# Kernel optimization log

Hardware: AMD Instinct MI355X
Metric: run time of the kernel (lower is better)

## Reference

```python
import jax, jax.numpy as jnp
import numpy as np

B, T, D, H, HD = 4, 2048, 1024, 16, 64
EPS = 1e-6


def _rotary_tables(seq_len, d_head):
    n = d_head // 4
    angular_freq = (1.0 / 1024) ** jnp.linspace(0, 1, n, dtype=jnp.float32)
    angular_freq = jnp.concatenate([angular_freq, jnp.zeros((n,), jnp.float32)])  # [d_head//2]
    theta = jnp.outer(jnp.arange(seq_len, dtype=jnp.float32), angular_freq)  # [T, d_head//2]
    return jnp.cos(theta), jnp.sin(theta)


def _apply_rotary(x, cos, sin):
    # x: [B, T, H, d]
    xf = x.astype(jnp.float32)
    x1, x2 = jnp.split(xf, 2, axis=-1)
    c = cos[None, :, None, :]
    s = sin[None, :, None, :]
    y1 = x1 * c + x2 * s
    y2 = -x1 * s + x2 * c
    return jnp.concatenate([y1, y2], axis=-1).astype(x.dtype)


def _rmsnorm(x, eps):
    return x * jax.lax.rsqrt(jnp.mean(x * x, axis=-1, keepdims=True) + eps)


def setup_inputs() -> dict:
    key = jax.random.key(0)
    ks = jax.random.split(key, 5)
    scale = 1.0 / np.sqrt(D)
    x = jax.random.normal(ks[0], (B, T, D), jnp.float32)
    wq = jax.random.normal(ks[1], (D, D), jnp.float32) * scale
    wk = jax.random.normal(ks[2], (D, D), jnp.float32) * scale
    wv = jax.random.normal(ks[3], (D, D), jnp.float32) * scale
    wo = jax.random.normal(ks[4], (D, D), jnp.float32) * scale
    mask = jnp.tril(jnp.ones((T, T), dtype=bool))  # causal
    return {"x": x, "wq": wq, "wk": wk, "wv": wv, "wo": wo, "mask": mask}


def reference(x, wq, wk, wv, wo, mask):
    # QKV projections (equinox Linear: y = x @ W.T)
    q = (x @ wq.T).reshape(B, T, H, HD)
    k = (x @ wk.T).reshape(B, T, H, HD)
    v = (x @ wv.T).reshape(B, T, H, HD)
    # QK-norm (RMS norm without weight)
    q = _rmsnorm(q, EPS)
    k = _rmsnorm(k, EPS)
    # Rotary embedding
    cos, sin = _rotary_tables(T, HD)
    q = _apply_rotary(q, cos, sin)
    k = _apply_rotary(k, cos, sin)
    # Attention
    scores = jnp.einsum('bshd,bthd->bhst', q, k) / jnp.sqrt(jnp.float32(HD))
    scores = jnp.where(mask[None, None, :, :], scores, -jnp.inf)
    weights = jax.nn.softmax(scores, axis=-1)
    out = jnp.einsum('bhst,bthd->bshd', weights, v)
    out = out.reshape(B, T, D)
    return out @ wo.T
```

## Files before the change

kernel.cpp:

```cpp
#include <hip/hip_runtime.h>
#include <hip/hip_bf16.h>
#include <math.h>

#define B_ 4
#define T_ 2048
#define D_ 1024
#define H_ 16
#define HD_ 64

typedef _Float16 f16x8 __attribute__((ext_vector_type(8)));
typedef _Float16 f16x4 __attribute__((ext_vector_type(4)));
typedef float f32x4 __attribute__((ext_vector_type(4)));

__device__ __forceinline__ void gload_lds16(const _Float16* g, _Float16* l) {
    __builtin_amdgcn_global_load_lds(
        (const __attribute__((address_space(1))) void*)g,
        (__attribute__((address_space(3))) void*)l,
        16, 0, 0);
}

__global__ __launch_bounds__(256) void castf(const float* __restrict__ in,
                                             _Float16* __restrict__ out, int n4) {
    const int i = blockIdx.x * 256 + threadIdx.x;
    if (i < n4) {
        const float4 v = ((const float4*)in)[i];
        f16x4 h = {(_Float16)v.x, (_Float16)v.y, (_Float16)v.z, (_Float16)v.w};
        ((f16x4*)out)[i] = h;
    }
}

__global__ __launch_bounds__(256) void castw(const float* __restrict__ a,
                                             const float* __restrict__ b,
                                             const float* __restrict__ c,
                                             const float* __restrict__ d,
                                             _Float16* __restrict__ oa,
                                             _Float16* __restrict__ ob,
                                             _Float16* __restrict__ oc,
                                             _Float16* __restrict__ od) {
    const int z = blockIdx.z;
    const float* in = (z == 0) ? a : (z == 1 ? b : (z == 2 ? c : d));
    _Float16* out = (z == 0) ? oa : (z == 1 ? ob : (z == 2 ? oc : od));
    const int i = blockIdx.x * 256 + threadIdx.x;
    const float4 v = ((const float4*)in)[i];
    f16x4 h = {(_Float16)v.x, (_Float16)v.y, (_Float16)v.z, (_Float16)v.w};
    ((f16x4*)out)[i] = h;
}

__global__ __launch_bounds__(256) void gemm_qkv(const _Float16* __restrict__ A,
                                                const _Float16* __restrict__ Wq,
                                                const _Float16* __restrict__ Wk,
                                                const _Float16* __restrict__ Wv,
                                                _Float16* __restrict__ qh,
                                                _Float16* __restrict__ kh,
                                                _Float16* __restrict__ vt) {
    constexpr int K = D_;
    const int z = blockIdx.z;
    const _Float16* W = (z == 0) ? Wq : (z == 1 ? Wk : Wv);
    __shared__ _Float16 As[128 * 32];
    __shared__ _Float16 Bs[128 * 32];
    const int tid = threadIdx.x;
    const int lane = tid & 63, w = tid >> 6;
    const int col = lane & 15, quad = lane >> 4;
    const int wm = w >> 1, wn = w & 1;
    const int row0 = blockIdx.y * 128, col0 = blockIdx.x * 128;
    const int sr = lane >> 2, sc = (lane & 3) * 8;

    f32x4 acc[4][4];
#pragma unroll
    for (int i = 0; i < 4; ++i)
#pragma unroll
        for (int j = 0; j < 4; ++j) acc[i][j] = (f32x4){0.f, 0.f, 0.f, 0.f};

    for (int kt = 0; kt < K / 32; ++kt) {
        const int k0 = kt * 32;
#pragma unroll
        for (int it = 0; it < 2; ++it) {
            const int rb = it * 64 + w * 16;
            gload_lds16(A + (size_t)(row0 + rb + sr) * K + k0 + sc, As + rb * 32);
            gload_lds16(W + (size_t)(col0 + rb + sr) * K + k0 + sc, Bs + rb * 32);
        }
        __syncthreads();
        f16x8 af[4], bf[4];
#pragma unroll
        for (int i = 0; i < 4; ++i) {
            af[i] = *(const f16x8*)&As[(wm * 64 + i * 16 + col) * 32 + quad * 8];
            bf[i] = *(const f16x8*)&Bs[(wn * 64 + i * 16 + col) * 32 + quad * 8];
        }
#pragma unroll
        for (int mi = 0; mi < 4; ++mi)
#pragma unroll
            for (int ni = 0; ni < 4; ++ni)
                acc[mi][ni] = __builtin_amdgcn_mfma_f32_16x16x32_f16(af[mi], bf[ni],
                                                                     acc[mi][ni], 0, 0, 0);
        __syncthreads();
    }

    if (z < 2) {
        _Float16* C = (z == 0) ? qh : kh;
        const float qscale = (z == 0) ? 0.18033688011112042f : 1.0f;
        const float fr = exp2f(-10.0f * (float)col * (1.0f / 15.0f));
#pragma unroll
        for (int mi = 0; mi < 4; ++mi) {
            float ssq[4];
#pragma unroll
            for (int r = 0; r < 4; ++r) {
                float t = 0.f;
#pragma unroll
                for (int ni = 0; ni < 4; ++ni) t += acc[mi][ni][r] * acc[mi][ni][r];
                ssq[r] = t;
            }
#pragma unroll
            for (int st = 1; st < 16; st <<= 1)
#pragma unroll
                for (int r = 0; r < 4; ++r) ssq[r] += __shfl_xor(ssq[r], st, 64);
            const int rowb = row0 + wm * 64 + mi * 16 + quad * 4;
#pragma unroll
            for (int r = 0; r < 4; ++r) {
                const float scl = rsqrtf(ssq[r] * (1.0f / 64.0f) + 1e-6f) * qscale;
                const int t = (rowb + r) & (T_ - 1);
                float s, c;
                sincosf((float)t * fr, &s, &c);
                const float x0 = acc[mi][0][r] * scl;
                const float x1 = acc[mi][1][r] * scl;
                const float x2 = acc[mi][2][r] * scl;
                const float x3 = acc[mi][3][r] * scl;
                const float y0 = fmaf(x0, c, x2 * s);
                const float y2 = fmaf(x2, c, -x0 * s);
                const size_t base = (size_t)(rowb + r) * D_ + col0 + wn * 64 + col;
                C[base + 0]  = (_Float16)y0;
                C[base + 16] = (_Float16)x1;
                C[base + 32] = (_Float16)y2;
                C[base + 48] = (_Float16)x3;
            }
        }
    } else {
        const int hh = blockIdx.x * 2 + wn;
#pragma unroll
        for (int mi = 0; mi < 4; ++mi) {
            const int row = row0 + wm * 64 + mi * 16 + quad * 4;
            const int bb = row >> 11;
            const int t0m = row & (T_ - 1);
#pragma unroll
            for (int ni = 0; ni < 4; ++ni) {
                const int d = ni * 16 + col;
                f16x4 pk = {(_Float16)acc[mi][ni][0], (_Float16)acc[mi][ni][1],
                            (_Float16)acc[mi][ni][2], (_Float16)acc[mi][ni][3]};
                *(f16x4*)&vt[((size_t)(bb * H_ + hh) * HD_ + d) * T_ + t0m] = pk;
            }
        }
    }
}

__global__ __launch_bounds__(256) void gemm_wo(const _Float16* __restrict__ A,
                                               const _Float16* __restrict__ W,
                                               float* __restrict__ C) {
    constexpr int K = D_, N = D_;
    __shared__ _Float16 As[128 * 32];
    __shared__ _Float16 Bs[128 * 32];
    const int tid = threadIdx.x;
    const int lane = tid & 63, w = tid >> 6;
    const int col = lane & 15, quad = lane >> 4;
    const int wm = w >> 1, wn = w & 1;
    const int row0 = blockIdx.y * 128, col0 = blockIdx.x * 128;
    const int sr = lane >> 2, sc = (lane & 3) * 8;

    f32x4 acc[4][4];
#pragma unroll
    for (int i = 0; i < 4; ++i)
#pragma unroll
        for (int j = 0; j < 4; ++j) acc[i][j] = (f32x4){0.f, 0.f, 0.f, 0.f};

    for (int kt = 0; kt < K / 32; ++kt) {
        const int k0 = kt * 32;
#pragma unroll
        for (int it = 0; it < 2; ++it) {
            const int rb = it * 64 + w * 16;
            gload_lds16(A + (size_t)(row0 + rb + sr) * K + k0 + sc, As + rb * 32);
            gload_lds16(W + (size_t)(col0 + rb + sr) * K + k0 + sc, Bs + rb * 32);
        }
        __syncthreads();
        f16x8 af[4], bf[4];
#pragma unroll
        for (int i = 0; i < 4; ++i) {
            af[i] = *(const f16x8*)&As[(wm * 64 + i * 16 + col) * 32 + quad * 8];
            bf[i] = *(const f16x8*)&Bs[(wn * 64 + i * 16 + col) * 32 + quad * 8];
        }
#pragma unroll
        for (int mi = 0; mi < 4; ++mi)
#pragma unroll
            for (int ni = 0; ni < 4; ++ni)
                acc[mi][ni] = __builtin_amdgcn_mfma_f32_16x16x32_f16(af[mi], bf[ni],
                                                                     acc[mi][ni], 0, 0, 0);
        __syncthreads();
    }
#pragma unroll
    for (int mi = 0; mi < 4; ++mi)
#pragma unroll
        for (int ni = 0; ni < 4; ++ni)
#pragma unroll
            for (int r = 0; r < 4; ++r)
                C[(size_t)(row0 + wm * 64 + mi * 16 + quad * 4 + r) * N +
                  col0 + wn * 64 + ni * 16 + col] = acc[mi][ni][r];
}

#define LDP 88

__global__ __launch_bounds__(512) void flash_mfma(const _Float16* __restrict__ qh,
                                                  const _Float16* __restrict__ kh,
                                                  const _Float16* __restrict__ vt,
                                                  _Float16* __restrict__ o) {
    __shared__ _Float16 Kl[64 * 64];
    __shared__ _Float16 Vl[64 * 64];
    __shared__ _Float16 Pl[8][16 * LDP];
    const int tid = threadIdx.x;
    const int lane = tid & 63, w = tid >> 6;
    const int col = lane & 15, quad = lane >> 4;
    const int bh = blockIdx.x, b = bh >> 4, h = bh & 15;
    const int srow = lane >> 3;
    const int schunk = (lane & 7) ^ srow;
    const int sw = col & 7;

    for (int phase = 0; phase < 2; ++phase) {
        const int qt = (phase == 0) ? (int)blockIdx.y : (15 - (int)blockIdx.y);
        const int q0 = qt * 128;

        const int tq = q0 + w * 16 + col;
        const _Float16* qp = qh + ((size_t)(b * T_ + tq) * H_ + h) * HD_ + quad * 8;
        const f16x8 qB0 = *(const f16x8*)(qp);
        const f16x8 qB1 = *(const f16x8*)(qp + 32);

        f32x4 oa[4];
#pragma unroll
        for (int i = 0; i < 4; ++i) oa[i] = (f32x4){0.f, 0.f, 0.f, 0.f};
        float l_ = 0.f;

        const int nkt = 2 * qt + 2;
        for (int kt = 0; kt < nkt; ++kt) {
            const int k0 = kt * 64;
            {
                const int r = w * 8 + srow;
                gload_lds16(kh + ((size_t)(b * T_ + k0 + r) * H_ + h) * HD_ + schunk * 8,
                            Kl + (w * 8) * 64);
                gload_lds16(vt + ((size_t)(b * H_ + h) * HD_ + r) * T_ + k0 + schunk * 8,
                            Vl + (w * 8) * 64);
            }
            __syncthreads();

            f32x4 s[4];
#pragma unroll
            for (int tn = 0; tn < 4; ++tn) {
                const _Float16* kp = &Kl[(tn * 16 + col) * 64];
                const f16x8 kA0 = *(const f16x8*)(kp + ((quad ^ sw) << 3));
                const f16x8 kA1 = *(const f16x8*)(kp + (((quad | 4) ^ sw) << 3));
                f32x4 a = (f32x4){0.f, 0.f, 0.f, 0.f};
                a = __builtin_amdgcn_mfma_f32_16x16x32_f16(kA0, qB0, a, 0, 0, 0);
                a = __builtin_amdgcn_mfma_f32_16x16x32_f16(kA1, qB1, a, 0, 0, 0);
                s[tn] = a;
            }

            if (k0 + 63 > q0 + w * 16) {
                const int qq = q0 + w * 16 + col;
#pragma unroll
                for (int tn = 0; tn < 4; ++tn)
#pragma unroll
                    for (int r = 0; r < 4; ++r) {
                        const int key = k0 + tn * 16 + quad * 4 + r;
                        if (key > qq) s[tn][r] = -1e30f;
                    }
            }

#pragma unroll
            for (int tn = 0; tn < 4; ++tn) {
                f16x4 pk;
#pragma unroll
                for (int r = 0; r < 4; ++r) {
                    const float p = exp2f(s[tn][r]);
                    l_ += p;
                    pk[r] = (_Float16)p;
                }
                *(f16x4*)&Pl[w][col * LDP + tn * 16 + quad * 4] = pk;
            }

            const f16x8 pA0 = *(const f16x8*)&Pl[w][col * LDP + quad * 8];
            const f16x8 pA1 = *(const f16x8*)&Pl[w][col * LDP + quad * 8 + 32];
#pragma unroll
            for (int tn = 0; tn < 4; ++tn) {
                const _Float16* vp = &Vl[(tn * 16 + col) * 64];
                const f16x8 vB0 = *(const f16x8*)(vp + ((quad ^ sw) << 3));
                const f16x8 vB1 = *(const f16x8*)(vp + (((quad | 4) ^ sw) << 3));
                oa[tn] = __builtin_amdgcn_mfma_f32_16x16x32_f16(pA0, vB0, oa[tn], 0, 0, 0);
                oa[tn] = __builtin_amdgcn_mfma_f32_16x16x32_f16(pA1, vB1, oa[tn], 0, 0, 0);
            }
            __syncthreads();
        }

        l_ += __shfl_xor(l_, 16, 64);
        l_ += __shfl_xor(l_, 32, 64);
        const float linv = 1.0f / l_;
        float inv[4];
#pragma unroll
        for (int r = 0; r < 4; ++r) inv[r] = __shfl(linv, quad * 4 + r, 64);
#pragma unroll
        for (int tn = 0; tn < 4; ++tn)
#pragma unroll
            for (int r = 0; r < 4; ++r)
                o[((size_t)(b * T_ + q0 + w * 16 + quad * 4 + r) * H_ + h) * HD_ + tn * 16 + col] =
                    (_Float16)(oa[tn][r] * inv[r]);
    }
}

extern "C" void kernel_launch(void* const* d_in, const int* in_sizes, int n_in,
                              void* d_out, int out_size, void* d_ws, size_t ws_size,
                              hipStream_t stream) {
    const float* x  = (const float*)d_in[0];
    const float* wq = (const float*)d_in[1];
    const float* wk = (const float*)d_in[2];
    const float* wv = (const float*)d_in[3];
    const float* wo = (const float*)d_in[4];
    float* out = (float*)d_out;

    const size_t NE = (size_t)B_ * T_ * D_;
    const size_t WE = (size_t)D_ * D_;
    _Float16* xh  = (_Float16*)d_ws;
    _Float16* qh  = xh + NE;
    _Float16* kh  = qh + NE;
    _Float16* vth = kh + NE;
    _Float16* oh  = vth + NE;
    _Float16* wqh = oh + NE;
    _Float16* wkh = wqh + WE;
    _Float16* wvh = wkh + WE;
    _Float16* woh = wvh + WE;

    castf<<<NE / 1024, 256, 0, stream>>>(x, xh, (int)(NE / 4));
    castw<<<dim3(WE / 1024, 1, 4), 256, 0, stream>>>(wq, wk, wv, wo,
                                                     wqh, wkh, wvh, woh);

    gemm_qkv<<<dim3(D_ / 128, (B_ * T_) / 128, 3), 256, 0, stream>>>(
        xh, wqh, wkh, wvh, qh, kh, vth);

    flash_mfma<<<dim3(B_ * H_, 8, 1), 512, 0, stream>>>(qh, kh, vth, oh);

    gemm_wo<<<dim3(D_ / 128, (B_ * T_) / 128, 1), 256, 0, stream>>>(oh, woh, out);
}
```

Before: 274.8 us.

## Rewrite QKV GEMM as 256x256 tile with double-buffered LDS ping-pong schedule

Measured after the change: 289.3 us. 1.05x slower.

```diff
diff --git a/kernel.cpp b/kernel.cpp
--- a/kernel.cpp
+++ b/kernel.cpp
@@ -46,61 +46,163 @@
     ((f16x4*)out)[i] = h;
 }
 
-__global__ __launch_bounds__(256) void gemm_qkv(const _Float16* __restrict__ A,
-                                                const _Float16* __restrict__ Wq,
-                                                const _Float16* __restrict__ Wk,
-                                                const _Float16* __restrict__ Wv,
-                                                _Float16* __restrict__ qh,
-                                                _Float16* __restrict__ kh,
-                                                _Float16* __restrict__ vt) {
-    constexpr int K = D_;
+
+#define PHASE_MID() \
+    __builtin_amdgcn_s_barrier(); \
+    asm volatile("s_waitcnt lgkmcnt(0)" ::: "memory"); \
+    __builtin_amdgcn_sched_barrier(0); \
+    __builtin_amdgcn_s_setprio(1)
+
+#define PHASE_END() \
+    __builtin_amdgcn_s_setprio(0); \
+    __builtin_amdgcn_s_barrier()
+
+#define VM_PHASE_END(N) \
+    __builtin_amdgcn_s_setprio(0); \
+    __builtin_amdgcn_sched_barrier(0); \
+    asm volatile("s_waitcnt vmcnt(" #N ")" ::: "memory"); \
+    __builtin_amdgcn_sched_barrier(0); \
+    __builtin_amdgcn_s_barrier()
+
+#define LOAD_A(AR, P, MH) { \
+    _Pragma("unroll") \
+    for (int i_ = 0; i_ < 4; ++i_) { \
+        AR[i_][0] = *(const f16x8*)&As[(P) * 16384 + rowA[MH][i_] + c0s]; \
+        AR[i_][1] = *(const f16x8*)&As[(P) * 16384 + rowA[MH][i_] + c1s]; \
+    } }
+
+#define LOAD_B(P, NH) { \
+    _Pragma("unroll") \
+    for (int j_ = 0; j_ < 2; ++j_) { \
+        bF[j_][0] = *(const f16x8*)&Bs[(P) * 16384 + rowB[2 * (NH) + j_] + c0s]; \
+        bF[j_][1] = *(const f16x8*)&Bs[(P) * 16384 + rowB[2 * (NH) + j_] + c1s]; \
+    } }
+
+#define MFMA_Q(AR, MB, NH) { \
+    _Pragma("unroll") \
+    for (int i_ = 0; i_ < 4; ++i_) { \
+        _Pragma("unroll") \
+        for (int j_ = 0; j_ < 2; ++j_) { \
+            f32x4& d_ = acc[(MB) + i_][2 * (NH) + j_]; \
+            d_ = __builtin_amdgcn_mfma_f32_16x16x32_f16(AR[i_][0], bF[j_][0], d_, 0, 0, 0); \
+            d_ = __builtin_amdgcn_mfma_f32_16x16x32_f16(AR[i_][1], bF[j_][1], d_, 0, 0, 0); \
+        } } }
+
+#define STAGE_A(P, T, HH) \
+    gload_lds16(Ap + (size_t)(row0 + (HH) * 128 + w8s) * 1024 + (T) * 64 + sch, \
+                &As[(P) * 16384 + (HH) * 8192 + (w << 9)]); \
+    gload_lds16(Ap + (size_t)(row0 + (HH) * 128 + 64 + w8s) * 1024 + (T) * 64 + sch, \
+                &As[(P) * 16384 + (HH) * 8192 + 4096 + (w << 9)])
+
+#define STAGE_B(P, T, HH) \
+    gload_lds16(Wp + (size_t)(col0 + (HH) * 128 + w8s) * 1024 + (T) * 64 + sch, \
+                &Bs[(P) * 16384 + (HH) * 8192 + (w << 9)]); \
+    gload_lds16(Wp + (size_t)(col0 + (HH) * 128 + 64 + w8s) * 1024 + (T) * 64 + sch, \
+                &Bs[(P) * 16384 + (HH) * 8192 + 4096 + (w << 9)])
+
+__global__ __launch_bounds__(512, 2) void gemm_qkv(const _Float16* __restrict__ A,
+                                                   const _Float16* __restrict__ Wq,
+                                                   const _Float16* __restrict__ Wk,
+                                                   const _Float16* __restrict__ Wv,
+                                                   _Float16* __restrict__ qh,
+                                                   _Float16* __restrict__ kh,
+                                                   _Float16* __restrict__ vt) {
     const int z = blockIdx.z;
-    const _Float16* W = (z == 0) ? Wq : (z == 1 ? Wk : Wv);
-    __shared__ _Float16 As[128 * 32];
-    __shared__ _Float16 Bs[128 * 32];
+    const _Float16* Wp = (z == 0) ? Wq : (z == 1 ? Wk : Wv);
+    const _Float16* Ap = A;
+    __shared__ _Float16 As[2 * 16384];
+    __shared__ _Float16 Bs[2 * 16384];
+
     const int tid = threadIdx.x;
     const int lane = tid & 63, w = tid >> 6;
     const int col = lane & 15, quad = lane >> 4;
-    const int wm = w >> 1, wn = w & 1;
-    const int row0 = blockIdx.y * 128, col0 = blockIdx.x * 128;
-    const int sr = lane >> 2, sc = (lane & 3) * 8;
-
-    f32x4 acc[4][4];
-#pragma unroll
-    for (int i = 0; i < 4; ++i)
+    const int wr = w >> 2, wc = w & 3;
+    const int row0 = blockIdx.y * 256, col0 = blockIdx.x * 256;
+
+    const int w8s = (w << 3) + (lane >> 3);
+    const int sch = (((lane & 7) ^ (lane >> 3)) << 3);
+
+    const int swz = col & 7;
+    const int c0s = ((quad ^ swz) << 3);
+    const int c1s = (((quad | 4) ^ swz) << 3);
+
+    int rowA[2][4], rowB[4];
+#pragma unroll
+    for (int i = 0; i < 4; ++i) {
+        rowA[0][i] = (wr * 128 + i * 16 + col) * 64;
+        rowA[1][i] = rowA[0][i] + 4096;
+        rowB[i]    = (wc * 64 + i * 16 + col) * 64;
+    }
+
+    f32x4 acc[8][4];
+#pragma unroll
+    for (int i = 0; i < 8; ++i)
 #pragma unroll
         for (int j = 0; j < 4; ++j) acc[i][j] = (f32x4){0.f, 0.f, 0.f, 0.f};
 
-    for (int kt = 0; kt < K / 32; ++kt) {
-        const int k0 = kt * 32;
-#pragma unroll
-        for (int it = 0; it < 2; ++it) {
-            const int rb = it * 64 + w * 16;
-            gload_lds16(A + (size_t)(row0 + rb + sr) * K + k0 + sc, As + rb * 32);
-            gload_lds16(W + (size_t)(col0 + rb + sr) * K + k0 + sc, Bs + rb * 32);
-        }
-        __syncthreads();
-        f16x8 af[4], bf[4];
-#pragma unroll
-        for (int i = 0; i < 4; ++i) {
-            af[i] = *(const f16x8*)&As[(wm * 64 + i * 16 + col) * 32 + quad * 8];
-            bf[i] = *(const f16x8*)&Bs[(wn * 64 + i * 16 + col) * 32 + quad * 8];
-        }
-#pragma unroll
-        for (int mi = 0; mi < 4; ++mi)
-#pragma unroll
-            for (int ni = 0; ni < 4; ++ni)
-                acc[mi][ni] = __builtin_amdgcn_mfma_f32_16x16x32_f16(af[mi], bf[ni],
-                                                                     acc[mi][ni], 0, 0, 0);
-        __syncthreads();
-    }
+    f16x8 aF[4][2], aG[4][2], bF[2][2];
+
+    STAGE_A(0, 0, 0); STAGE_A(0, 0, 1);
+    STAGE_B(0, 0, 0); STAGE_B(0, 0, 1);
+    STAGE_A(1, 1, 0); STAGE_A(1, 1, 1);
+    __builtin_amdgcn_sched_barrier(0);
+    asm volatile("s_waitcnt vmcnt(4)" ::: "memory");
+    __builtin_amdgcn_sched_barrier(0);
+    __builtin_amdgcn_s_barrier();
+
+    for (int it = 0; it < 7; ++it) {
+        const int c1 = 2 * it + 1, n0 = 2 * it + 2, n1 = 2 * it + 3;
+        LOAD_A(aF, 0, 0); LOAD_B(0, 0);
+        STAGE_B(1, c1, 0);
+        PHASE_MID(); MFMA_Q(aF, 0, 0); PHASE_END();
+        LOAD_A(aG, 0, 1);
+        STAGE_B(1, c1, 1);
+        PHASE_MID(); MFMA_Q(aG, 4, 0); PHASE_END();
+        LOAD_B(0, 1);
+        STAGE_A(0, n0, 0);
+        PHASE_MID(); MFMA_Q(aG, 4, 1); PHASE_END();
+        STAGE_A(0, n0, 1);
+        PHASE_MID(); MFMA_Q(aF, 0, 1);
+        VM_PHASE_END(4);
+        LOAD_A(aF, 1, 0); LOAD_B(1, 0);
+        STAGE_B(0, n0, 0);
+        PHASE_MID(); MFMA_Q(aF, 0, 0); PHASE_END();
+        LOAD_A(aG, 1, 1);
+        STAGE_B(0, n0, 1);
+        PHASE_MID(); MFMA_Q(aG, 4, 0); PHASE_END();
+        LOAD_B(1, 1);
+        STAGE_A(1, n1, 0);
+        PHASE_MID(); MFMA_Q(aG, 4, 1); PHASE_END();
+        STAGE_A(1, n1, 1);
+        PHASE_MID(); MFMA_Q(aF, 0, 1);
+        VM_PHASE_END(4);
+    }
+
+    LOAD_A(aF, 0, 0); LOAD_B(0, 0);
+    STAGE_B(1, 15, 0);
+    PHASE_MID(); MFMA_Q(aF, 0, 0); PHASE_END();
+    LOAD_A(aG, 0, 1);
+    STAGE_B(1, 15, 1);
+    PHASE_MID(); MFMA_Q(aG, 4, 0); PHASE_END();
+    LOAD_B(0, 1);
+    PHASE_MID(); MFMA_Q(aG, 4, 1); PHASE_END();
+    PHASE_MID(); MFMA_Q(aF, 0, 1);
+    VM_PHASE_END(0);
+    LOAD_A(aF, 1, 0); LOAD_B(1, 0);
+    PHASE_MID(); MFMA_Q(aF, 0, 0); PHASE_END();
+    LOAD_A(aG, 1, 1);
+    PHASE_MID(); MFMA_Q(aG, 4, 0); PHASE_END();
+    LOAD_B(1, 1);
+    PHASE_MID(); MFMA_Q(aG, 4, 1); PHASE_END();
+    PHASE_MID(); MFMA_Q(aF, 0, 1);
+    __builtin_amdgcn_s_setprio(0);
 
     if (z < 2) {
         _Float16* C = (z == 0) ? qh : kh;
         const float qscale = (z == 0) ? 0.18033688011112042f : 1.0f;
         const float fr = exp2f(-10.0f * (float)col * (1.0f / 15.0f));
 #pragma unroll
-        for (int mi = 0; mi < 4; ++mi) {
+        for (int mi = 0; mi < 8; ++mi) {
             float ssq[4];
 #pragma unroll
             for (int r = 0; r < 4; ++r) {
@@ -113,7 +215,7 @@
             for (int st = 1; st < 16; st <<= 1)
 #pragma unroll
                 for (int r = 0; r < 4; ++r) ssq[r] += __shfl_xor(ssq[r], st, 64);
-            const int rowb = row0 + wm * 64 + mi * 16 + quad * 4;
+            const int rowb = row0 + wr * 128 + mi * 16 + quad * 4;
 #pragma unroll
             for (int r = 0; r < 4; ++r) {
                 const float scl = rsqrtf(ssq[r] * (1.0f / 64.0f) + 1e-6f) * qscale;
@@ -126,7 +228,7 @@
                 const float x3 = acc[mi][3][r] * scl;
                 const float y0 = fmaf(x0, c, x2 * s);
                 const float y2 = fmaf(x2, c, -x0 * s);
-                const size_t base = (size_t)(rowb + r) * D_ + col0 + wn * 64 + col;
+                const size_t base = (size_t)(rowb + r) * D_ + col0 + wc * 64 + col;
                 C[base + 0]  = (_Float16)y0;
                 C[base + 16] = (_Float16)x1;
                 C[base + 32] = (_Float16)y2;
@@ -134,10 +236,10 @@
             }
         }
     } else {
-        const int hh = blockIdx.x * 2 + wn;
-#pragma unroll
-        for (int mi = 0; mi < 4; ++mi) {
-            const int row = row0 + wm * 64 + mi * 16 + quad * 4;
+        const int hh = blockIdx.x * 4 + wc;
+#pragma unroll
+        for (int mi = 0; mi < 8; ++mi) {
+            const int row = row0 + wr * 128 + mi * 16 + quad * 4;
             const int bb = row >> 11;
             const int t0m = row & (T_ - 1);
 #pragma unroll
@@ -335,7 +437,7 @@
     castw<<<dim3(WE / 1024, 1, 4), 256, 0, stream>>>(wq, wk, wv, wo,
                                                      wqh, wkh, wvh, woh);
 
-    gemm_qkv<<<dim3(D_ / 128, (B_ * T_) / 128, 3), 256, 0, stream>>>(
+    gemm_qkv<<<dim3(D_ / 256, (B_ * T_) / 256, 3), 512, 0, stream>>>(
         xh, wqh, wkh, wvh, qh, kh, vth);
 
     flash_mfma<<<dim3(B_ * H_, 8, 1), 512, 0, stream>>>(qh, kh, vth, oh);
```

## Double-buffer K/V tiles in flash attention with async prefetch and setprio

Applied to the files above, without the earlier changes.

New measurement: 275.3 us. Within noise of the previous version (+0.2%).

```diff
diff --git a/kernel.cpp b/kernel.cpp
--- a/kernel.cpp
+++ b/kernel.cpp
@@ -209,8 +209,8 @@
                                                   const _Float16* __restrict__ kh,
                                                   const _Float16* __restrict__ vt,
                                                   _Float16* __restrict__ o) {
-    __shared__ _Float16 Kl[64 * 64];
-    __shared__ _Float16 Vl[64 * 64];
+    __shared__ _Float16 Kl[2][64 * 64];
+    __shared__ _Float16 Vl[2][64 * 64];
     __shared__ _Float16 Pl[8][16 * LDP];
     const int tid = threadIdx.x;
     const int lane = tid & 63, w = tid >> 6;
@@ -219,6 +219,10 @@
     const int srow = lane >> 3;
     const int schunk = (lane & 7) ^ srow;
     const int sw = col & 7;
+    const int rstg = w * 8 + srow;
+
+    const _Float16* kbase = kh + ((size_t)b * T_ * H_ + (size_t)h) * HD_;
+    const _Float16* vbase = vt + ((size_t)(b * H_ + h)) * (size_t)HD_ * T_;
 
     for (int phase = 0; phase < 2; ++phase) {
         const int qt = (phase == 0) ? (int)blockIdx.y : (15 - (int)blockIdx.y);
@@ -235,21 +239,32 @@
         float l_ = 0.f;
 
         const int nkt = 2 * qt + 2;
+
+        gload_lds16(kbase + (size_t)(0 + rstg) * H_ * HD_ + schunk * 8,
+                    &Kl[0][(w * 8) * 64]);
+        gload_lds16(vbase + (size_t)rstg * T_ + 0 + schunk * 8,
+                    &Vl[0][(w * 8) * 64]);
+        __builtin_amdgcn_sched_barrier(0);
+        asm volatile("s_waitcnt vmcnt(0)" ::: "memory");
+        __builtin_amdgcn_sched_barrier(0);
+        __builtin_amdgcn_s_barrier();
+
         for (int kt = 0; kt < nkt; ++kt) {
             const int k0 = kt * 64;
-            {
-                const int r = w * 8 + srow;
-                gload_lds16(kh + ((size_t)(b * T_ + k0 + r) * H_ + h) * HD_ + schunk * 8,
-                            Kl + (w * 8) * 64);
-                gload_lds16(vt + ((size_t)(b * H_ + h) * HD_ + r) * T_ + k0 + schunk * 8,
-                            Vl + (w * 8) * 64);
-            }
-            __syncthreads();
+            const int cur = kt & 1;
+
+            if (kt + 1 < nkt) {
+                gload_lds16(kbase + (size_t)(k0 + 64 + rstg) * H_ * HD_ + schunk * 8,
+                            &Kl[cur ^ 1][(w * 8) * 64]);
+                gload_lds16(vbase + (size_t)rstg * T_ + k0 + 64 + schunk * 8,
+                            &Vl[cur ^ 1][(w * 8) * 64]);
+            }
 
             f32x4 s[4];
+            __builtin_amdgcn_s_setprio(1);
 #pragma unroll
             for (int tn = 0; tn < 4; ++tn) {
-                const _Float16* kp = &Kl[(tn * 16 + col) * 64];
+                const _Float16* kp = &Kl[cur][(tn * 16 + col) * 64];
                 const f16x8 kA0 = *(const f16x8*)(kp + ((quad ^ sw) << 3));
                 const f16x8 kA1 = *(const f16x8*)(kp + (((quad | 4) ^ sw) << 3));
                 f32x4 a = (f32x4){0.f, 0.f, 0.f, 0.f};
@@ -257,6 +272,7 @@
                 a = __builtin_amdgcn_mfma_f32_16x16x32_f16(kA1, qB1, a, 0, 0, 0);
                 s[tn] = a;
             }
+            __builtin_amdgcn_s_setprio(0);
 
             if (k0 + 63 > q0 + w * 16) {
                 const int qq = q0 + w * 16 + col;
@@ -283,15 +299,21 @@
 
             const f16x8 pA0 = *(const f16x8*)&Pl[w][col * LDP + quad * 8];
             const f16x8 pA1 = *(const f16x8*)&Pl[w][col * LDP + quad * 8 + 32];
+            __builtin_amdgcn_s_setprio(1);
 #pragma unroll
             for (int tn = 0; tn < 4; ++tn) {
-                const _Float16* vp = &Vl[(tn * 16 + col) * 64];
+                const _Float16* vp = &Vl[cur][(tn * 16 + col) * 64];
                 const f16x8 vB0 = *(const f16x8*)(vp + ((quad ^ sw) << 3));
                 const f16x8 vB1 = *(const f16x8*)(vp + (((quad | 4) ^ sw) << 3));
                 oa[tn] = __builtin_amdgcn_mfma_f32_16x16x32_f16(pA0, vB0, oa[tn], 0, 0, 0);
                 oa[tn] = __builtin_amdgcn_mfma_f32_16x16x32_f16(pA1, vB1, oa[tn], 0, 0, 0);
             }
-            __syncthreads();
+            __builtin_amdgcn_s_setprio(0);
+
+            __builtin_amdgcn_sched_barrier(0);
+            asm volatile("s_waitcnt vmcnt(0)" ::: "memory");
+            __builtin_amdgcn_sched_barrier(0);
+            __builtin_amdgcn_s_barrier();
         }
 
         l_ += __shfl_xor(l_, 16, 64);
```
